# Performance work log

Measured on AMD Instinct MI355X. Metric: run time of the kernel, lower is better.

## Reference

```python
import jax, jax.numpy as jnp
import numpy as np

N_NODES = 16384
N_EDGES = 65536
N_GRAPHS = 64
HID = 768
D = 256       # gnn_hidden_dim == gnn_out_features
HEADS = 4
EPS_LN = 1e-5


def setup_inputs() -> dict:
    key = jax.random.key(0)
    ks = jax.random.split(key, 20)
    s = 0.02
    inp = {
        'text_cls': jax.random.normal(ks[0], (N_GRAPHS, HID), jnp.float32),
        'node_x': jax.random.normal(ks[1], (N_NODES, HID), jnp.float32),
        'node_proj_w': jax.random.normal(ks[2], (HID, D), jnp.float32) * s,
        'node_proj_b': jnp.zeros((D,), jnp.float32),
        # TransformerConv params, stacked over 2 layers. Q/K/V: D -> heads*D
        'Wq': jax.random.normal(ks[3], (2, D, HEADS * D), jnp.float32) * s,
        'bq': jnp.zeros((2, HEADS * D), jnp.float32),
        'Wk': jax.random.normal(ks[4], (2, D, HEADS * D), jnp.float32) * s,
        'bk': jnp.zeros((2, HEADS * D), jnp.float32),
        'Wv': jax.random.normal(ks[5], (2, D, HEADS * D), jnp.float32) * s,
        'bv': jnp.zeros((2, HEADS * D), jnp.float32),
        # root/skip connection: D -> D
        'Ws': jax.random.normal(ks[6], (2, D, D), jnp.float32) * s,
        'bs': jnp.zeros((2, D), jnp.float32),
        # index 0 = gnn_norms[0], index 1 = gnn_last_norm
        'norm_gamma': jnp.ones((2, D), jnp.float32),
        'norm_beta': jnp.zeros((2, D), jnp.float32),
        'clf_w': jax.random.normal(ks[7], (2 * D + HID, 1), jnp.float32) * s,
        'clf_b': jnp.zeros((1,), jnp.float32),
        'edge_index': jax.random.randint(ks[8], (2, N_EDGES), 0, N_NODES, jnp.int32),
        'batch_ids': jnp.sort(jax.random.randint(ks[9], (N_NODES,), 0, N_GRAPHS, jnp.int32)),
    }
    return inp


def _layernorm(x, g, b):
    mu = x.mean(-1, keepdims=True)
    var = ((x - mu) ** 2).mean(-1, keepdims=True)
    return (x - mu) * jax.lax.rsqrt(var + EPS_LN) * g + b


def _transformer_conv(x, src, dst, Wq, bq, Wk, bk, Wv, bv, Ws, bs):
    # PyG TransformerConv: heads=4, concat=False (mean over heads), root_weight=True
    N = x.shape[0]
    q = (x @ Wq + bq).reshape(N, HEADS, D)
    k = (x @ Wk + bk).reshape(N, HEADS, D)
    v = (x @ Wv + bv).reshape(N, HEADS, D)
    qe, ke, ve = q[dst], k[src], v[src]                 # [E, H, D]
    score = (qe * ke).sum(-1) / jnp.sqrt(jnp.float32(D))  # [E, H]
    m = jax.ops.segment_max(score, dst, num_segments=N)
    m = jnp.where(jnp.isfinite(m), m, 0.0)
    ex = jnp.exp(score - m[dst])
    den = jax.ops.segment_sum(ex, dst, num_segments=N)
    alpha = ex / (den[dst] + 1e-16)                     # softmax over in-edges
    agg = jax.ops.segment_sum(alpha[..., None] * ve, dst, num_segments=N)  # [N,H,D]
    return agg.mean(axis=1) + x @ Ws + bs


def reference(text_cls, node_x, node_proj_w, node_proj_b, Wq, bq, Wk, bk, Wv, bv,
              Ws, bs, norm_gamma, norm_beta, clf_w, clf_b, edge_index, batch_ids):
    B = text_cls.shape[0]
    src, dst = edge_index[0], edge_index[1]

    # claim-relevance reweighting (cosine similarity)
    tex = text_cls[batch_ids]                            # [N, 768]
    num = (tex * node_x).sum(-1)
    den = jnp.linalg.norm(tex, axis=-1) * jnp.linalg.norm(node_x, axis=-1)
    rel = num / jnp.maximum(den, 1e-8)
    nf = node_x * rel[:, None]

    x = nf @ node_proj_w + node_proj_b                   # [N, 256]
    for i in range(2):
        h = _transformer_conv(x, src, dst, Wq[i], bq[i], Wk[i], bk[i],
                              Wv[i], bv[i], Ws[i], bs[i])
        if i < 1:
            h = _layernorm(h + x, norm_gamma[i], norm_beta[i])   # residual + LN
        else:
            h = _layernorm(h, norm_gamma[i], norm_beta[i])       # last norm
        x = jax.nn.relu(h)

    # structural mean pool
    counts = jax.ops.segment_sum(jnp.ones((x.shape[0],), x.dtype), batch_ids,
                                 num_segments=B)
    pool_struct = jax.ops.segment_sum(x, batch_ids, num_segments=B) \
        / jnp.maximum(counts, 1.0)[:, None]

    # semantic claim-attention pool (attn_proj is Identity since out==hidden)
    tproj = tex @ node_proj_w + node_proj_b
    scores = (x * tproj).sum(-1)                         # [N]
    ex = jnp.exp(scores)                                 # raw exp, as in source
    denom = jax.ops.segment_sum(ex, batch_ids, num_segments=B)
    aw = ex / (denom[batch_ids] + 1e-8)
    pool_sem = jax.ops.segment_sum(x * aw[:, None], batch_ids, num_segments=B)

    combined = jnp.concatenate([pool_struct, pool_sem, text_cls], axis=-1)
    logits = (combined @ clf_w + clf_b)[:, 0]            # [B]
    return logits
```

## Files before the change

kernel.cpp:

```cpp
#include <hip/hip_runtime.h>

#define N_NODES 16384
#define N_EDGES 65536
#define N_GRAPHS 64
#define HID 768
#define DDIM 256
#define HEADS 4

typedef __attribute__((ext_vector_type(8))) short bf16x8;
typedef __attribute__((ext_vector_type(4))) float f32x4;
typedef __attribute__((ext_vector_type(8))) unsigned short u16x8;

#define GLL(SRC, DST) __builtin_amdgcn_global_load_lds( \
    (const __attribute__((address_space(1))) void*)(SRC), \
    (__attribute__((address_space(3))) void*)(DST), 16, 0, 0)

__device__ __forceinline__ float wave_reduce_sum(float v) {
#pragma unroll
    for (int off = 32; off; off >>= 1) v += __shfl_xor(v, off);
    return v;
}

__device__ __forceinline__ unsigned short f2bf(float f) {
    unsigned u = __float_as_uint(f);
    return (unsigned short)((u + 0x7fffu + ((u >> 16) & 1u)) >> 16);
}
__device__ __forceinline__ float bf2f(unsigned short h) {
    return __uint_as_float((unsigned)h << 16);
}

__global__ __launch_bounds__(256) void relnf_kernel(
        const float* __restrict__ text, const float* __restrict__ nodex,
        const int* __restrict__ bid, unsigned short* __restrict__ nfs) {
    int n = blockIdx.x, t = threadIdx.x;
    const float* xr = nodex + (size_t)n * HID;
    const float* tr = text + (size_t)bid[n] * HID;
    float xv[3];
    float num = 0.f, tt = 0.f, xx = 0.f;
#pragma unroll
    for (int j = 0; j < 3; j++) {
        int c = t + j * 256;
        float a = xr[c], b = tr[c];
        xv[j] = a; num += a * b; tt += b * b; xx += a * a;
    }
    num = wave_reduce_sum(num);
    tt = wave_reduce_sum(tt);
    xx = wave_reduce_sum(xx);
    __shared__ float s0[4], s1[4], s2[4];
    int lane = t & 63, wv = t >> 6;
    if (lane == 0) { s0[wv] = num; s1[wv] = tt; s2[wv] = xx; }
    __syncthreads();
    num = s0[0] + s0[1] + s0[2] + s0[3];
    tt  = s1[0] + s1[1] + s1[2] + s1[3];
    xx  = s2[0] + s2[1] + s2[2] + s2[3];
    float r = num / fmaxf(sqrtf(tt) * sqrtf(xx), 1e-8f);
    unsigned short* o = nfs + (size_t)n * 1536;
#pragma unroll
    for (int j = 0; j < 3; j++) {
        int c = t + j * 256;
        o[c] = f2bf(xv[j] * r);
    }
}

__global__ void wconv_kernel(const float* __restrict__ W, unsigned short* __restrict__ out,
                             int K, int N) {
    int k = blockIdx.x * 256 + threadIdx.x;
    int n = blockIdx.y;
    if (k >= K) return;
    float a = W[(size_t)k * N + n];
    unsigned short h = f2bf(a);
    unsigned short l = f2bf(a - bf2f(h));
    size_t o = (size_t)n * (3 * K);
    out[o + k] = h;
    out[o + K + k] = h;
    out[o + 2 * K + k] = l;
}

__global__ void wprep_kernel(const float* __restrict__ Wq, const float* __restrict__ Wk,
                             const float* __restrict__ Wv, const float* __restrict__ Ws,
                             const float* __restrict__ bq, const float* __restrict__ bk,
                             const float* __restrict__ bv, const float* __restrict__ bs,
                             unsigned short* __restrict__ Wall, float* __restrict__ ballY) {
    __shared__ float red[4];
    int L = blockIdx.y;
    const float* Wk_ = Wk + (size_t)L * DDIM * 1024;
    const float* Wv_ = Wv + (size_t)L * DDIM * 1024;
    const float* Ws_ = Ws + (size_t)L * DDIM * DDIM;
    const float* bq_ = bq + L * 1024;
    const float* bv_ = bv + L * 1024;
    const float* bs_ = bs + L * DDIM;
    unsigned short* Wl = Wall + (size_t)L * 2304 * 256;
    float* bl = ballY + L * 2304;
    int n = blockIdx.x, t = threadIdx.x;
    int lane = t & 63, wv = t >> 6;
    if (n < 1024) {
        Wl[(size_t)(1024 + n) * 256 + t] = f2bf(Wv_[(size_t)t * 1024 + n]);
        if (t == 0) bl[1024 + n] = bv_[n];
    } else if (n < 1280) {
        int col = n - 1024;
        Wl[(size_t)(2048 + col) * 256 + t] = f2bf(Ws_[(size_t)t * 256 + col]);
        if (t == 0) bl[2048 + col] = bs_[col];
    } else {
        int m = n - 1280; int h = m >> 8, b = m & 255;
        float v = Wk_[(size_t)b * 1024 + h * 256 + t] * bq_[h * 256 + t];
        v = wave_reduce_sum(v);
        if (lane == 0) red[wv] = v;
        __syncthreads();
        if (t == 0) bl[m] = red[0] + red[1] + red[2] + red[3];
    }
}

__global__ __launch_bounds__(256, 2) void mker_f32(
        const float* __restrict__ WA, const float* __restrict__ WB,
        unsigned short* __restrict__ Wall) {
    __shared__ unsigned short As_[128 * 64];
    __shared__ unsigned short Bs_[128 * 64];
    const int tid = threadIdx.x;
    const int lane = tid & 63, wave = tid >> 6;
    const int wm = wave >> 1, wn = wave & 1;
    const int row0 = blockIdx.y * 128, col0 = blockIdx.x * 128;
    const int z = blockIdx.z, L = z >> 2, h = z & 3;
    const float* Aq = WA + (size_t)L * DDIM * 1024;
    const float* Ak = WB + (size_t)L * DDIM * 1024;
    unsigned short* Wl = Wall + (size_t)L * 2304 * 256;
    const int l15 = lane & 15, l16 = lane >> 4;
    f32x4 acc[4][4] = {};
    int sr = tid >> 1, scc = (tid & 1) * 32;
    for (int k0 = 0; k0 < 256; k0 += 64) {
        __syncthreads();
        {
            const float* pa = Aq + (size_t)(row0 + sr) * 1024 + h * 256 + k0 + scc;
            const float* pb = Ak + (size_t)(col0 + sr) * 1024 + h * 256 + k0 + scc;
            unsigned short* da = As_ + sr * 64 + scc;
            unsigned short* db = Bs_ + sr * 64 + scc;
#pragma unroll
            for (int j = 0; j < 8; j++) {
                float4 va = ((const float4*)pa)[j];
                float4 vb2 = ((const float4*)pb)[j];
                ((ushort4*)da)[j] = make_ushort4(f2bf(va.x), f2bf(va.y), f2bf(va.z), f2bf(va.w));
                ((ushort4*)db)[j] = make_ushort4(f2bf(vb2.x), f2bf(vb2.y), f2bf(vb2.z), f2bf(vb2.w));
            }
        }
        __syncthreads();
#pragma unroll
        for (int kk = 0; kk < 2; kk++) {
            bf16x8 af[4], bfr[4];
#pragma unroll
            for (int f = 0; f < 4; f++) {
                af[f]  = *(const bf16x8*)(As_ + ((wm * 64 + f * 16 + l15) * 64 + kk * 32 + l16 * 8));
                bfr[f] = *(const bf16x8*)(Bs_ + ((wn * 64 + f * 16 + l15) * 64 + kk * 32 + l16 * 8));
            }
#pragma unroll
            for (int fi = 0; fi < 4; fi++)
#pragma unroll
                for (int fj = 0; fj < 4; fj++)
                    acc[fi][fj] = __builtin_amdgcn_mfma_f32_16x16x32_bf16(
                        af[fi], bfr[fj], acc[fi][fj], 0, 0, 0);
        }
    }
#pragma unroll
    for (int fj = 0; fj < 4; fj++) {
        int cc = col0 + wn * 64 + fj * 16 + l15;
#pragma unroll
        for (int fi = 0; fi < 4; fi++) {
            int rbase = row0 + wm * 64 + fi * 16 + l16 * 4;
#pragma unroll
            for (int r = 0; r < 4; r++)
                Wl[(size_t)(h * 256 + rbase + r) * 256 + cc] = f2bf(acc[fi][fj][r]);
        }
    }
}

__device__ __forceinline__ void swz_block(int& bx, int& by) {
    int nwg = gridDim.x * gridDim.y;
    int lin = blockIdx.y * gridDim.x + blockIdx.x;
    int qd = nwg >> 3, rr = nwg & 7;
    int xcd = lin & 7, j = lin >> 3;
    int wg = (xcd < rr ? xcd * (qd + 1) : rr * (qd + 1) + (xcd - rr) * qd) + j;
    bx = wg % gridDim.x;
    by = wg / gridDim.x;
}

__global__ __launch_bounds__(256, 4) void gemm_proj64(
        const unsigned short* __restrict__ A, const unsigned short* __restrict__ B,
        const float* __restrict__ bias, float* __restrict__ x,
        unsigned short* __restrict__ xb) {
    __shared__ unsigned short As[2][4096];
    __shared__ unsigned short Bs[2][4096];
    int bx, by; swz_block(bx, by);
    const int tid = threadIdx.x;
    const int lane = tid & 63, wave = tid >> 6;
    const int wm = wave >> 1, wn = wave & 1;
    const int row0 = by * 64, col0 = bx * 64;
    const int l15 = lane & 15, l16 = lane >> 4;
    f32x4 acc[2][2] = {};
    const char* Ac = (const char*)A;
    const char* Bc = (const char*)B;

#define PSTAGE(BUF, T) do { \
    int k_ = (T) * 128; \
    _Pragma("unroll") \
    for (int i_ = 0; i_ < 2; i_++) { \
        int o_ = i_ * 4096 + tid * 16; \
        int r_ = o_ >> 7, cb_ = o_ & 127; \
        int cs_ = cb_ ^ ((r_ & 7) << 4); \
        GLL(Ac + (size_t)(row0 + r_) * 3072 + k_ + cs_, (char*)As[BUF] + o_); \
        GLL(Bc + (size_t)(col0 + r_) * 4608 + k_ + cs_, (char*)Bs[BUF] + o_); \
    } } while (0)

#define PCOMPUTE(BUF) do { \
    _Pragma("unroll") \
    for (int kk = 0; kk < 2; kk++) { \
        bf16x8 af[2], bfr[2]; \
        _Pragma("unroll") \
        for (int f = 0; f < 2; f++) { \
            int rowa_ = wm * 32 + f * 16 + l15; \
            int qba_ = (kk * 64 + l16 * 16) ^ ((rowa_ & 7) << 4); \
            af[f]  = *(const bf16x8*)((const char*)As[BUF] + rowa_ * 128 + qba_); \
            int rowb_ = wn * 32 + f * 16 + l15; \
            int qbb_ = (kk * 64 + l16 * 16) ^ ((rowb_ & 7) << 4); \
            bfr[f] = *(const bf16x8*)((const char*)Bs[BUF] + rowb_ * 128 + qbb_); \
        } \
        _Pragma("unroll") \
        for (int fi = 0; fi < 2; fi++) \
            _Pragma("unroll") \
            for (int fj = 0; fj < 2; fj++) \
                acc[fi][fj] = __builtin_amdgcn_mfma_f32_16x16x32_bf16( \
                    af[fi], bfr[fj], acc[fi][fj], 0, 0, 0); \
    } } while (0)

    PSTAGE(0, 0);
    __syncthreads();
    for (int t = 0; t < 12; t += 2) {
        PSTAGE(1, t + 1);
        PCOMPUTE(0); __syncthreads();
        if (t + 2 < 12) PSTAGE(0, t + 2);
        PCOMPUTE(1); __syncthreads();
    }
#undef PSTAGE
#undef PCOMPUTE
    float* smemf = (float*)&As[0][0];
#pragma unroll
    for (int fj = 0; fj < 2; fj++) {
        int cl = wn * 32 + fj * 16 + l15;
        float bb = bias[col0 + cl];
#pragma unroll
        for (int fi = 0; fi < 2; fi++)
#pragma unroll
            for (int r = 0; r < 4; r++) {
                int rl = wm * 32 + fi * 16 + l16 * 4 + r;
                int c16 = cl >> 2;
                smemf[rl * 64 + ((c16 ^ (rl & 15)) << 2) + (cl & 3)] = acc[fi][fj][r] + bb;
            }
    }
    __syncthreads();
    int rl = tid >> 2, q = tid & 3;
#pragma unroll
    for (int i = 0; i < 4; i++) {
        int c16 = q * 4 + i;
        float4 v4 = *(const float4*)&smemf[rl * 64 + ((c16 ^ (rl & 15)) << 2)];
        *(float4*)(x + (size_t)(row0 + rl) * 256 + col0 + c16 * 4) = v4;
        *(ushort4*)(xb + (size_t)(row0 + rl) * 256 + col0 + c16 * 4) =
            make_ushort4(f2bf(v4.x), f2bf(v4.y), f2bf(v4.z), f2bf(v4.w));
    }
}

__global__ __launch_bounds__(256, 6) void gemm_yvs64(
        const unsigned short* __restrict__ A, const unsigned short* __restrict__ B,
        const float* __restrict__ ball,
        unsigned short* __restrict__ Yb, unsigned short* __restrict__ vb,
        unsigned short* __restrict__ hb) {
    __shared__ unsigned short smem[12288];
    unsigned short* As = smem;
    unsigned short* Bs = smem + 4096;
    int bx, by; swz_block(bx, by);
    const int tid = threadIdx.x;
    const int lane = tid & 63, wave = tid >> 6;
    const int wm = wave >> 1, wn = wave & 1;
    const int row0 = by * 64, col0 = bx * 128;
    const int l15 = lane & 15, l16 = lane >> 4;
    f32x4 acc[2][4] = {};
    const char* Ac = (const char*)A;
    const char* Bc = (const char*)B;

    for (int k0 = 0; k0 < 256; k0 += 64) {
        __syncthreads();
#pragma unroll
        for (int i = 0; i < 2; i++) {
            int o = i * 4096 + tid * 16;
            int r = o >> 7, cb = o & 127;
            GLL(Ac + (size_t)(row0 + r) * 512 + k0 * 2 + (cb ^ ((r & 7) << 4)), (char*)As + o);
        }
#pragma unroll
        for (int i = 0; i < 4; i++) {
            int o = i * 4096 + tid * 16;
            int r = o >> 7, cb = o & 127;
            GLL(Bc + (size_t)(col0 + r) * 512 + k0 * 2 + (cb ^ ((r & 7) << 4)), (char*)Bs + o);
        }
        __syncthreads();
#pragma unroll
        for (int kk = 0; kk < 2; kk++) {
            bf16x8 af[2], bfr[4];
#pragma unroll
            for (int f = 0; f < 2; f++) {
                int row = wm * 32 + f * 16 + l15;
                int qb_ = (kk * 64 + l16 * 16) ^ ((row & 7) << 4);
                af[f] = *(const bf16x8*)((const char*)As + row * 128 + qb_);
            }
#pragma unroll
            for (int f = 0; f < 4; f++) {
                int row = wn * 64 + f * 16 + l15;
                int qb_ = (kk * 64 + l16 * 16) ^ ((row & 7) << 4);
                bfr[f] = *(const bf16x8*)((const char*)Bs + row * 128 + qb_);
            }
#pragma unroll
            for (int fi = 0; fi < 2; fi++)
#pragma unroll
                for (int fj = 0; fj < 4; fj++)
                    acc[fi][fj] = __builtin_amdgcn_mfma_f32_16x16x32_bf16(
                        af[fi], bfr[fj], acc[fi][fj], 0, 0, 0);
        }
    }
    __syncthreads();
#pragma unroll
    for (int fj = 0; fj < 4; fj++) {
        int cl = wn * 64 + fj * 16 + l15;
        float bb = ball[col0 + cl];
#pragma unroll
        for (int fi = 0; fi < 2; fi++)
#pragma unroll
            for (int r = 0; r < 4; r++) {
                int rl = wm * 32 + fi * 16 + l16 * 4 + r;
                int chunk = (cl >> 3) ^ (rl & 15);
                smem[rl * 128 + chunk * 8 + (cl & 7)] = f2bf(acc[fi][fj][r] + bb);
            }
    }
    __syncthreads();
    int rl = tid >> 2, part = tid & 3;
    unsigned short* dstp;
    if (col0 < 1024)      dstp = Yb + (size_t)(row0 + rl) * 1024 + col0 + part * 32;
    else if (col0 < 2048) dstp = vb + (size_t)(row0 + rl) * 1024 + (col0 - 1024) + part * 32;
    else                  dstp = hb + (size_t)(row0 + rl) * 256 + (col0 - 2048) + part * 32;
#pragma unroll
    for (int i = 0; i < 4; i++) {
        int chunk = (part * 4 + i) ^ (rl & 15);
        ((u16x8*)dstp)[i] = *(const u16x8*)(smem + rl * 128 + chunk * 8);
    }
}

__global__ __launch_bounds__(256) void tp_kernel(
        const float* __restrict__ text, const float* __restrict__ Wp,
        const float* __restrict__ bp, float* __restrict__ tp64) {
    __shared__ float trow[768];
    int g = blockIdx.x, t = threadIdx.x;
#pragma unroll
    for (int j = 0; j < 3; j++) trow[t + j * 256] = text[(size_t)g * 768 + t + j * 256];
    __syncthreads();
    float acc = bp[t];
#pragma unroll 4
    for (int k = 0; k < 768; k++) acc += trow[k] * Wp[(size_t)k * 256 + t];
    tp64[(size_t)g * 256 + t] = acc;
}

__global__ void hist_kernel(const int* __restrict__ dst, int* __restrict__ cnt) {
    int e = blockIdx.x * 256 + threadIdx.x;
    if (e < N_EDGES) atomicAdd(&cnt[dst[e]], 1);
}

__global__ void scan_kernel(const int* __restrict__ cnt, int* __restrict__ base,
                            int* __restrict__ cursor) {
    int t = threadIdx.x;
    int s = 0;
    for (int i = 0; i < 64; i++) s += cnt[t * 64 + i];
    __shared__ int pref[256];
    pref[t] = s;
    __syncthreads();
    if (t == 0) {
        int a = 0;
        for (int i = 0; i < 256; i++) { int v = pref[i]; pref[i] = a; a += v; }
    }
    __syncthreads();
    int run = pref[t];
    for (int i = 0; i < 64; i++) {
        base[t * 64 + i] = run;
        cursor[t * 64 + i] = run;
        run += cnt[t * 64 + i];
    }
}

__global__ void scatter_kernel(const int* __restrict__ src, const int* __restrict__ dst,
                               int* __restrict__ cursor, int* __restrict__ esrc) {
    int e = blockIdx.x * 256 + threadIdx.x;
    if (e < N_EDGES) {
        int d = dst[e];
        int pos = atomicAdd(&cursor[d], 1);
        esrc[pos] = src[e];
    }
}

__global__ void gbounds_kernel(const int* __restrict__ bid, int* __restrict__ gstart) {
    int g = threadIdx.x;
    if (g > N_GRAPHS) return;
    int lo = 0, hi = N_NODES;
    while (lo < hi) { int mid = (lo + hi) >> 1; if (bid[mid] < g) lo = mid + 1; else hi = mid; }
    gstart[g] = lo;
}

template<bool RESID, bool WXB>
__global__ __launch_bounds__(256) void agg_norm_fused(
        const unsigned short* __restrict__ vb, const unsigned short* __restrict__ Yb,
        const int* __restrict__ base, const int* __restrict__ cnt,
        const int* __restrict__ esrc, const unsigned short* __restrict__ hb,
        float* __restrict__ x, const unsigned short* __restrict__ xin,
        unsigned short* __restrict__ xout,
        const float* __restrict__ gamma, const float* __restrict__ beta) {
    __shared__ float hacc[4][256];
    __shared__ float tmp[4];
    int n = (blockIdx.x & 7) * (N_NODES >> 3) + (blockIdx.x >> 3);
    int tid = threadIdx.x, lane = tid & 63, h = tid >> 6;
    int start = base[n], deg = cnt[n];

    ushort4 ya = ((const ushort4*)(Yb + (size_t)n * 1024 + h * 256))[lane];
    float y0 = bf2f(ya.x), y1 = bf2f(ya.y), y2 = bf2f(ya.z), y3 = bf2f(ya.w);

    float m0 = -1e30f, den0 = 0.f, m1 = -1e30f, den1 = 0.f;
    float4 acc0 = {0.f, 0.f, 0.f, 0.f}, acc1 = {0.f, 0.f, 0.f, 0.f};
    ushort4 xsA = {0, 0, 0, 0}, vvA = {0, 0, 0, 0};
    ushort4 xsB = {0, 0, 0, 0}, vvB = {0, 0, 0, 0};
    if (deg > 0) {
        int s = esrc[start];
        xsA = ((const ushort4*)(xin + (size_t)s * 256))[lane];
        vvA = ((const ushort4*)(vb + (size_t)s * 1024 + h * 256))[lane];
    }
    if (deg > 1) {
        int s = esrc[start + 1];
        xsB = ((const ushort4*)(xin + (size_t)s * 256))[lane];
        vvB = ((const ushort4*)(vb + (size_t)s * 1024 + h * 256))[lane];
    }
    for (int i = 0; i < deg; i += 2) {
        ushort4 xsA_n = xsA, vvA_n = vvA, xsB_n = xsB, vvB_n = vvB;
        if (i + 2 < deg) {
            int s = esrc[start + i + 2];
            xsA_n = ((const ushort4*)(xin + (size_t)s * 256))[lane];
            vvA_n = ((const ushort4*)(vb + (size_t)s * 1024 + h * 256))[lane];
        }
        if (i + 3 < deg) {
            int s = esrc[start + i + 3];
            xsB_n = ((const ushort4*)(xin + (size_t)s * 256))[lane];
            vvB_n = ((const ushort4*)(vb + (size_t)s * 1024 + h * 256))[lane];
        }
        float p0 = y0 * bf2f(xsA.x) + y1 * bf2f(xsA.y)
                 + y2 * bf2f(xsA.z) + y3 * bf2f(xsA.w);
        float p1 = y0 * bf2f(xsB.x) + y1 * bf2f(xsB.y)
                 + y2 * bf2f(xsB.z) + y3 * bf2f(xsB.w);
#pragma unroll
        for (int off = 32; off; off >>= 1) {
            p0 += __shfl_xor(p0, off);
            p1 += __shfl_xor(p1, off);
        }
        p0 *= 0.0625f; p1 *= 0.0625f;
        if (p0 > m0) {
            float sc_ = __expf(m0 - p0);
            den0 = den0 * sc_ + 1.0f;
            acc0.x = acc0.x * sc_ + bf2f(vvA.x);
            acc0.y = acc0.y * sc_ + bf2f(vvA.y);
            acc0.z = acc0.z * sc_ + bf2f(vvA.z);
            acc0.w = acc0.w * sc_ + bf2f(vvA.w);
            m0 = p0;
        } else {
            float a = __expf(p0 - m0);
            den0 += a;
            acc0.x += a * bf2f(vvA.x); acc0.y += a * bf2f(vvA.y);
            acc0.z += a * bf2f(vvA.z); acc0.w += a * bf2f(vvA.w);
        }
        if (i + 1 < deg) {
            if (p1 > m1) {
                float sc_ = __expf(m1 - p1);
                den1 = den1 * sc_ + 1.0f;
                acc1.x = acc1.x * sc_ + bf2f(vvB.x);
                acc1.y = acc1.y * sc_ + bf2f(vvB.y);
                acc1.z = acc1.z * sc_ + bf2f(vvB.z);
                acc1.w = acc1.w * sc_ + bf2f(vvB.w);
                m1 = p1;
            } else {
                float a = __expf(p1 - m1);
                den1 += a;
                acc1.x += a * bf2f(vvB.x); acc1.y += a * bf2f(vvB.y);
                acc1.z += a * bf2f(vvB.z); acc1.w += a * bf2f(vvB.w);
            }
        }
        xsA = xsA_n; vvA = vvA_n; xsB = xsB_n; vvB = vvB_n;
    }
    float mm = fmaxf(m0, m1);
    float e0 = __expf(m0 - mm), e1 = __expf(m1 - mm);
    float den = den0 * e0 + den1 * e1;
    float4 acc;
    acc.x = acc0.x * e0 + acc1.x * e1;
    acc.y = acc0.y * e0 + acc1.y * e1;
    acc.z = acc0.z * e0 + acc1.z * e1;
    acc.w = acc0.w * e0 + acc1.w * e1;
    float inv_den = 0.25f / (den + 1e-16f);
    acc.x *= inv_den; acc.y *= inv_den; acc.z *= inv_den; acc.w *= inv_den;
    ((float4*)&hacc[h][lane * 4])[0] = acc;
    __syncthreads();

    int c = tid;
    float val = hacc[0][c] + hacc[1][c] + hacc[2][c] + hacc[3][c]
              + bf2f(hb[(size_t)n * 256 + c]);
    if (RESID) val += x[(size_t)n * 256 + c];

    float s1 = wave_reduce_sum(val);
    if (lane == 0) tmp[h] = s1;
    __syncthreads();
    float mu = (tmp[0] + tmp[1] + tmp[2] + tmp[3]) * (1.0f / 256.0f);
    __syncthreads();
    float d = val - mu;
    float s2 = wave_reduce_sum(d * d);
    if (lane == 0) tmp[h] = s2;
    __syncthreads();
    float inv = rsqrtf((tmp[0] + tmp[1] + tmp[2] + tmp[3]) * (1.0f / 256.0f) + 1e-5f);
    float o = fmaxf(d * inv * gamma[c] + beta[c], 0.f);
    x[(size_t)n * 256 + c] = o;
    if (WXB) xout[(size_t)n * 256 + c] = f2bf(o);
}

__global__ __launch_bounds__(256) void pool_seg(
        const float* __restrict__ x, const float* __restrict__ tp,
        const int* __restrict__ gstart, float* __restrict__ pstruct,
        float* __restrict__ psem, float* __restrict__ semden) {
    int g = blockIdx.x >> 2, q = blockIdx.x & 3;
    int s0 = gstart[g], s1 = gstart[g + 1];
    int chunk = (s1 - s0 + 3) >> 2;
    int a = s0 + q * chunk, b = min(a + chunk, s1);
    int wave = threadIdx.x >> 6, lane = threadIdx.x & 63;
    float4 tv = ((const float4*)(tp + (size_t)g * 256))[lane];
    float4 acc = {0.f, 0.f, 0.f, 0.f};
    float4 accs = {0.f, 0.f, 0.f, 0.f};
    float esum = 0.f;
    for (int n = a + wave; n < b; n += 4) {
        float4 xv = ((const float4*)(x + (size_t)n * 256))[lane];
        float p = wave_reduce_sum(xv.x * tv.x + xv.y * tv.y + xv.z * tv.z + xv.w * tv.w);
        float e = __expf(p);
        esum += e;
        acc.x += xv.x; acc.y += xv.y; acc.z += xv.z; acc.w += xv.w;
        accs.x += e * xv.x; accs.y += e * xv.y; accs.z += e * xv.z; accs.w += e * xv.w;
    }
    __shared__ float sacc[4][256];
    __shared__ float sacc2[4][256];
    __shared__ float tse[4];
    ((float4*)&sacc[wave][lane * 4])[0] = acc;
    ((float4*)&sacc2[wave][lane * 4])[0] = accs;
    if (lane == 0) tse[wave] = esum;
    __syncthreads();
    int c = threadIdx.x;
    float v = sacc[0][c] + sacc[1][c] + sacc[2][c] + sacc[3][c];
    float v2 = sacc2[0][c] + sacc2[1][c] + sacc2[2][c] + sacc2[3][c];
    atomicAdd(&pstruct[(size_t)g * 256 + c], v);
    atomicAdd(&psem[(size_t)g * 256 + c], v2);
    if (threadIdx.x == 0)
        atomicAdd(&semden[g], tse[0] + tse[1] + tse[2] + tse[3]);
}

__global__ void clf_kernel(const float* __restrict__ pstruct, const float* __restrict__ psem,
                           const float* __restrict__ semden,
                           const int* __restrict__ gstart, const float* __restrict__ text,
                           const float* __restrict__ w, const float* __restrict__ b,
                           float* __restrict__ out) {
    int g = blockIdx.x * 4 + (threadIdx.x >> 6);
    int lane = threadIdx.x & 63;
    float invc = 1.0f / fmaxf((float)(gstart[g + 1] - gstart[g]), 1.0f);
    float invs = 1.0f / (semden[g] + 1e-8f);
    float acc = 0.f;
#pragma unroll
    for (int i = 0; i < 4; i++) { int c = lane + i * 64; acc += pstruct[(size_t)g * 256 + c] * invc * w[c]; }
#pragma unroll
    for (int i = 0; i < 4; i++) { int c = lane + i * 64; acc += psem[(size_t)g * 256 + c] * invs * w[256 + c]; }
#pragma unroll
    for (int i = 0; i < 12; i++) { int c = lane + i * 64; acc += text[(size_t)g * 768 + c] * w[512 + c]; }
    acc = wave_reduce_sum(acc);
    if (lane == 0) out[g] = acc + b[0];
}

extern "C" void kernel_launch(void* const* d_in, const int* in_sizes, int n_in,
                              void* d_out, int out_size, void* d_ws, size_t ws_size,
                              hipStream_t stream) {
    const float* text  = (const float*)d_in[0];
    const float* nodex = (const float*)d_in[1];
    const float* Wp    = (const float*)d_in[2];
    const float* bp    = (const float*)d_in[3];
    const float* Wq    = (const float*)d_in[4];
    const float* bq    = (const float*)d_in[5];
    const float* Wk    = (const float*)d_in[6];
    const float* bk    = (const float*)d_in[7];
    const float* Wv    = (const float*)d_in[8];
    const float* bv    = (const float*)d_in[9];
    const float* Ws    = (const float*)d_in[10];
    const float* bs    = (const float*)d_in[11];
    const float* gamma = (const float*)d_in[12];
    const float* beta  = (const float*)d_in[13];
    const float* clfw  = (const float*)d_in[14];
    const float* clfb  = (const float*)d_in[15];
    const int*   eidx  = (const int*)d_in[16];
    const int*   bid   = (const int*)d_in[17];
    const int* src = eidx;
    const int* dst = eidx + N_EDGES;
    float* out = (float*)d_out;

    float* x     = (float*)d_ws;
    float* tp64  = x + (size_t)N_NODES * 256;
    float* pstruct = tp64 + 64 * 256;
    float* psem  = pstruct + 64 * 256;
    float* semden = psem + 64 * 256;
    float* ballY = semden + 64;
    int* esrc    = (int*)(ballY + 2 * 2304);
    int* cnt     = esrc + N_EDGES;
    int* base    = cnt + N_NODES;
    int* cursor  = base + N_NODES;
    int* gstart  = cursor + N_NODES;
    unsigned short* Yb   = (unsigned short*)(gstart + 80);
    unsigned short* vb   = Yb + (size_t)N_NODES * 1024;
    unsigned short* hb   = vb + (size_t)N_NODES * 1024;
    unsigned short* xb   = hb + (size_t)N_NODES * 256;
    unsigned short* xb2  = xb + (size_t)N_NODES * 256;
    unsigned short* Wall = xb2 + (size_t)N_NODES * 256;
    unsigned short* Wps  = Wall + (size_t)2 * 2304 * 256;
    unsigned short* nfs = Yb;

    relnf_kernel<<<N_NODES, 256, 0, stream>>>(text, nodex, bid, nfs);
    hipMemsetAsync(cnt, 0, N_NODES * sizeof(int), stream);
    hist_kernel<<<N_EDGES / 256, 256, 0, stream>>>(dst, cnt);
    scan_kernel<<<1, 256, 0, stream>>>(cnt, base, cursor);
    scatter_kernel<<<N_EDGES / 256, 256, 0, stream>>>(src, dst, cursor, esrc);
    gbounds_kernel<<<1, 128, 0, stream>>>(bid, gstart);

    wconv_kernel<<<dim3(HID / 256, DDIM), 256, 0, stream>>>(Wp, Wps, HID, DDIM);
    wprep_kernel<<<dim3(2304, 2), 256, 0, stream>>>(Wq, Wk, Wv, Ws, bq, bk, bv, bs,
                                                    Wall, ballY);
    mker_f32<<<dim3(2, 2, 8), 256, 0, stream>>>(Wk, Wq, Wall);

    gemm_proj64<<<dim3(DDIM / 64, N_NODES / 64), 256, 0, stream>>>(nfs, Wps, bp, x, xb);
    tp_kernel<<<N_GRAPHS, 256, 0, stream>>>(text, Wp, bp, tp64);

    for (int i = 0; i < 2; i++) {
        const unsigned short* xin = (i == 0) ? xb : xb2;
        gemm_yvs64<<<dim3(18, N_NODES / 64), 256, 0, stream>>>(
            xin, Wall + (size_t)i * 2304 * 256, ballY + i * 2304, Yb, vb, hb);
        if (i == 0)
            agg_norm_fused<true, true><<<N_NODES, 256, 0, stream>>>(
                vb, Yb, base, cnt, esrc, hb, x, xin, xb2, gamma, beta);
        else
            agg_norm_fused<false, false><<<N_NODES, 256, 0, stream>>>(
                vb, Yb, base, cnt, esrc, hb, x, xin, xb2, gamma + 256, beta + 256);
    }

    hipMemsetAsync(pstruct, 0, (size_t)(64 * 256 * 2 + 64) * sizeof(float), stream);
    pool_seg<<<N_GRAPHS * 4, 256, 0, stream>>>(x, tp64, gstart, pstruct, psem, semden);
    clf_kernel<<<N_GRAPHS / 4, 256, 0, stream>>>(pstruct, psem, semden, gstart, text,
                                                 clfw, clfb, out);
}
```

Measured before the change: 336.7 us.

## Merge weight-prep, text projection and memsets into one launch; fold histogram into relnf

Replaces the wconv, wprep, mker, tp kernels and two memsets with a single prep_mega launch that branches on block index. The edge-degree histogram moves into relnf_kernel (each node block adds four edges' counts), and the graph-bounds search moves into scan_kernel. This cuts the number of launches and their small-kernel tail overhead. The cost is a heterogeneous mega-kernel whose register and LDS footprint is set by the MFMA branch, which may limit occupancy for the simple branches.

```diff
diff --git a/kernel.cpp b/kernel.cpp
--- a/kernel.cpp
+++ b/kernel.cpp
@@ -31,8 +31,10 @@
 
 __global__ __launch_bounds__(256) void relnf_kernel(
         const float* __restrict__ text, const float* __restrict__ nodex,
-        const int* __restrict__ bid, unsigned short* __restrict__ nfs) {
+        const int* __restrict__ bid, const int* __restrict__ dst,
+        unsigned short* __restrict__ nfs, int* __restrict__ cnt) {
     int n = blockIdx.x, t = threadIdx.x;
+    if (t < 4) atomicAdd(&cnt[dst[4 * n + t]], 1);
     const float* xr = nodex + (size_t)n * HID;
     const float* tr = text + (size_t)bid[n] * HID;
     float xv[3];
@@ -62,112 +64,163 @@
     }
 }
 
-__global__ void wconv_kernel(const float* __restrict__ W, unsigned short* __restrict__ out,
-                             int K, int N) {
-    int k = blockIdx.x * 256 + threadIdx.x;
-    int n = blockIdx.y;
-    if (k >= K) return;
-    float a = W[(size_t)k * N + n];
-    unsigned short h = f2bf(a);
-    unsigned short l = f2bf(a - bf2f(h));
-    size_t o = (size_t)n * (3 * K);
-    out[o + k] = h;
-    out[o + K + k] = h;
-    out[o + 2 * K + k] = l;
-}
-
-__global__ void wprep_kernel(const float* __restrict__ Wq, const float* __restrict__ Wk,
-                             const float* __restrict__ Wv, const float* __restrict__ Ws,
-                             const float* __restrict__ bq, const float* __restrict__ bk,
-                             const float* __restrict__ bv, const float* __restrict__ bs,
-                             unsigned short* __restrict__ Wall, float* __restrict__ ballY) {
-    __shared__ float red[4];
-    int L = blockIdx.y;
-    const float* Wk_ = Wk + (size_t)L * DDIM * 1024;
-    const float* Wv_ = Wv + (size_t)L * DDIM * 1024;
-    const float* Ws_ = Ws + (size_t)L * DDIM * DDIM;
-    const float* bq_ = bq + L * 1024;
-    const float* bv_ = bv + L * 1024;
-    const float* bs_ = bs + L * DDIM;
-    unsigned short* Wl = Wall + (size_t)L * 2304 * 256;
-    float* bl = ballY + L * 2304;
-    int n = blockIdx.x, t = threadIdx.x;
-    int lane = t & 63, wv = t >> 6;
-    if (n < 1024) {
-        Wl[(size_t)(1024 + n) * 256 + t] = f2bf(Wv_[(size_t)t * 1024 + n]);
-        if (t == 0) bl[1024 + n] = bv_[n];
-    } else if (n < 1280) {
-        int col = n - 1024;
-        Wl[(size_t)(2048 + col) * 256 + t] = f2bf(Ws_[(size_t)t * 256 + col]);
-        if (t == 0) bl[2048 + col] = bs_[col];
-    } else {
-        int m = n - 1280; int h = m >> 8, b = m & 255;
-        float v = Wk_[(size_t)b * 1024 + h * 256 + t] * bq_[h * 256 + t];
-        v = wave_reduce_sum(v);
-        if (lane == 0) red[wv] = v;
-        __syncthreads();
-        if (t == 0) bl[m] = red[0] + red[1] + red[2] + red[3];
-    }
-}
-
-__global__ __launch_bounds__(256, 2) void mker_f32(
-        const float* __restrict__ WA, const float* __restrict__ WB,
-        unsigned short* __restrict__ Wall) {
+__global__ __launch_bounds__(256, 2) void prep_mega(
+        const float* __restrict__ Wp, const float* __restrict__ Wq,
+        const float* __restrict__ Wk, const float* __restrict__ Wv,
+        const float* __restrict__ Ws, const float* __restrict__ bq,
+        const float* __restrict__ bk, const float* __restrict__ bv,
+        const float* __restrict__ bs, const float* __restrict__ text,
+        const float* __restrict__ bp,
+        unsigned short* __restrict__ Wps, unsigned short* __restrict__ Wall,
+        float* __restrict__ ballY, float* __restrict__ tp64,
+        int* __restrict__ cnt, float* __restrict__ pzero) {
     __shared__ unsigned short As_[128 * 64];
     __shared__ unsigned short Bs_[128 * 64];
-    const int tid = threadIdx.x;
-    const int lane = tid & 63, wave = tid >> 6;
-    const int wm = wave >> 1, wn = wave & 1;
-    const int row0 = blockIdx.y * 128, col0 = blockIdx.x * 128;
-    const int z = blockIdx.z, L = z >> 2, h = z & 3;
-    const float* Aq = WA + (size_t)L * DDIM * 1024;
-    const float* Ak = WB + (size_t)L * DDIM * 1024;
-    unsigned short* Wl = Wall + (size_t)L * 2304 * 256;
-    const int l15 = lane & 15, l16 = lane >> 4;
-    f32x4 acc[4][4] = {};
-    int sr = tid >> 1, scc = (tid & 1) * 32;
-    for (int k0 = 0; k0 < 256; k0 += 64) {
+    const int b = blockIdx.x, t = threadIdx.x;
+    if (b < 768) {
+        int k = (b % 3) * 256 + t, n = b / 3;
+        float a = Wp[(size_t)k * 256 + n];
+        unsigned short h = f2bf(a), l = f2bf(a - bf2f(h));
+        size_t o = (size_t)n * 2304;
+        Wps[o + k] = h; Wps[o + 768 + k] = h; Wps[o + 1536 + k] = l;
+    } else if (b < 5376) {
+        float* red = (float*)As_;
+        int m = b - 768;
+        int n = m % 2304, L = m / 2304;
+        const float* Wk_ = Wk + (size_t)L * DDIM * 1024;
+        const float* Wv_ = Wv + (size_t)L * DDIM * 1024;
+        const float* Ws_ = Ws + (size_t)L * DDIM * DDIM;
+        const float* bq_ = bq + L * 1024;
+        const float* bv_ = bv + L * 1024;
+        const float* bs_ = bs + L * DDIM;
+        unsigned short* Wl = Wall + (size_t)L * 2304 * 256;
+        float* bl = ballY + L * 2304;
+        int lane = t & 63, wv = t >> 6;
+        if (n < 1024) {
+            Wl[(size_t)(1024 + n) * 256 + t] = f2bf(Wv_[(size_t)t * 1024 + n]);
+            if (t == 0) bl[1024 + n] = bv_[n];
+        } else if (n < 1280) {
+            int col = n - 1024;
+            Wl[(size_t)(2048 + col) * 256 + t] = f2bf(Ws_[(size_t)t * 256 + col]);
+            if (t == 0) bl[2048 + col] = bs_[col];
+        } else {
+            int mm = n - 1280; int h = mm >> 8, bcol = mm & 255;
+            float v = Wk_[(size_t)bcol * 1024 + h * 256 + t] * bq_[h * 256 + t];
+            v = wave_reduce_sum(v);
+            if (lane == 0) red[wv] = v;
+            __syncthreads();
+            if (t == 0) bl[mm] = red[0] + red[1] + red[2] + red[3];
+        }
+    } else if (b < 5408) {
+        int m = b - 5376;
+        const int bx = m & 1, by = (m >> 1) & 1, z = m >> 2;
+        const int L = z >> 2, h = z & 3;
+        const int lane = t & 63, wave = t >> 6;
+        const int wm = wave >> 1, wn = wave & 1;
+        const int row0 = by * 128, col0 = bx * 128;
+        const float* Aq = Wk + (size_t)L * DDIM * 1024;
+        const float* Ak = Wq + (size_t)L * DDIM * 1024;
+        unsigned short* Wl = Wall + (size_t)L * 2304 * 256;
+        const int l15 = lane & 15, l16 = lane >> 4;
+        f32x4 acc[4][4] = {};
+        int sr = t >> 1, scc = (t & 1) * 32;
+        for (int k0 = 0; k0 < 256; k0 += 64) {
+            __syncthreads();
+            {
+                const float* pa = Aq + (size_t)(row0 + sr) * 1024 + h * 256 + k0 + scc;
+                const float* pb = Ak + (size_t)(col0 + sr) * 1024 + h * 256 + k0 + scc;
+                unsigned short* da = As_ + sr * 64 + scc;
+                unsigned short* db = Bs_ + sr * 64 + scc;
+#pragma unroll
+                for (int j = 0; j < 8; j++) {
+                    float4 va = ((const float4*)pa)[j];
+                    float4 vb2 = ((const float4*)pb)[j];
+                    ((ushort4*)da)[j] = make_ushort4(f2bf(va.x), f2bf(va.y), f2bf(va.z), f2bf(va.w));
+                    ((ushort4*)db)[j] = make_ushort4(f2bf(vb2.x), f2bf(vb2.y), f2bf(vb2.z), f2bf(vb2.w));
+                }
+            }
+            __syncthreads();
+#pragma unroll
+            for (int kk = 0; kk < 2; kk++) {
+                bf16x8 af[4], bfr[4];
+#pragma unroll
+                for (int f = 0; f < 4; f++) {
+                    af[f]  = *(const bf16x8*)(As_ + ((wm * 64 + f * 16 + l15) * 64 + kk * 32 + l16 * 8));
+                    bfr[f] = *(const bf16x8*)(Bs_ + ((wn * 64 + f * 16 + l15) * 64 + kk * 32 + l16 * 8));
+                }
+#pragma unroll
+                for (int fi = 0; fi < 4; fi++)
+#pragma unroll
+                    for (int fj = 0; fj < 4; fj++)
+                        acc[fi][fj] = __builtin_amdgcn_mfma_f32_16x16x32_bf16(
+                            af[fi], bfr[fj], acc[fi][fj], 0, 0, 0);
+            }
+        }
+#pragma unroll
+        for (int fj = 0; fj < 4; fj++) {
+            int cc = col0 + wn * 64 + fj * 16 + l15;
+#pragma unroll
+            for (int fi = 0; fi < 4; fi++) {
+                int rbase = row0 + wm * 64 + fi * 16 + l16 * 4;
+#pragma unroll
+                for (int r = 0; r < 4; r++)
+                    Wl[(size_t)(h * 256 + rbase + r) * 256 + cc] = f2bf(acc[fi][fj][r]);
+            }
+        }
+    } else if (b < 5472) {
+        float* trow = (float*)As_;
+        int g = b - 5408;
+#pragma unroll
+        for (int j = 0; j < 3; j++) trow[t + j * 256] = text[(size_t)g * 768 + t + j * 256];
         __syncthreads();
-        {
-            const float* pa = Aq + (size_t)(row0 + sr) * 1024 + h * 256 + k0 + scc;
-            const float* pb = Ak + (size_t)(col0 + sr) * 1024 + h * 256 + k0 + scc;
-            unsigned short* da = As_ + sr * 64 + scc;
-            unsigned short* db = Bs_ + sr * 64 + scc;
-#pragma unroll
-            for (int j = 0; j < 8; j++) {
-                float4 va = ((const float4*)pa)[j];
-                float4 vb2 = ((const float4*)pb)[j];
-                ((ushort4*)da)[j] = make_ushort4(f2bf(va.x), f2bf(va.y), f2bf(va.z), f2bf(va.w));
-                ((ushort4*)db)[j] = make_ushort4(f2bf(vb2.x), f2bf(vb2.y), f2bf(vb2.z), f2bf(vb2.w));
-            }
-        }
-        __syncthreads();
-#pragma unroll
-        for (int kk = 0; kk < 2; kk++) {
-            bf16x8 af[4], bfr[4];
-#pragma unroll
-            for (int f = 0; f < 4; f++) {
-                af[f]  = *(const bf16x8*)(As_ + ((wm * 64 + f * 16 + l15) * 64 + kk * 32 + l16 * 8));
-                bfr[f] = *(const bf16x8*)(Bs_ + ((wn * 64 + f * 16 + l15) * 64 + kk * 32 + l16 * 8));
-            }
-#pragma unroll
-            for (int fi = 0; fi < 4; fi++)
-#pragma unroll
-                for (int fj = 0; fj < 4; fj++)
-                    acc[fi][fj] = __builtin_amdgcn_mfma_f32_16x16x32_bf16(
-                        af[fi], bfr[fj], acc[fi][fj], 0, 0, 0);
-        }
-    }
-#pragma unroll
-    for (int fj = 0; fj < 4; fj++) {
-        int cc = col0 + wn * 64 + fj * 16 + l15;
-#pragma unroll
-        for (int fi = 0; fi < 4; fi++) {
-            int rbase = row0 + wm * 64 + fi * 16 + l16 * 4;
-#pragma unroll
-            for (int r = 0; r < 4; r++)
-                Wl[(size_t)(h * 256 + rbase + r) * 256 + cc] = f2bf(acc[fi][fj][r]);
-        }
+        float acc = bp[t];
+#pragma unroll 4
+        for (int k = 0; k < 768; k++) acc += trow[k] * Wp[(size_t)k * 256 + t];
+        tp64[(size_t)g * 256 + t] = acc;
+    } else if (b < 5488) {
+        int i = (b - 5472) * 1024 + t * 4;
+        ((int4*)(cnt + i))[0] = make_int4(0, 0, 0, 0);
+    } else {
+        int i = (b - 5488) * 1024 + t * 4;
+        if (i < 32832)
+            ((float4*)(pzero + i))[0] = make_float4(0.f, 0.f, 0.f, 0.f);
+    }
+}
+
+__global__ void scan_kernel(const int* __restrict__ cnt, int* __restrict__ base,
+                            int* __restrict__ cursor, const int* __restrict__ bid,
+                            int* __restrict__ gstart) {
+    int t = threadIdx.x;
+    if (t <= 64) {
+        int lo = 0, hi = N_NODES;
+        while (lo < hi) { int mid = (lo + hi) >> 1; if (bid[mid] < t) lo = mid + 1; else hi = mid; }
+        gstart[t] = lo;
+    }
+    int s = 0;
+    for (int i = 0; i < 64; i++) s += cnt[t * 64 + i];
+    __shared__ int pref[256];
+    pref[t] = s;
+    __syncthreads();
+    if (t == 0) {
+        int a = 0;
+        for (int i = 0; i < 256; i++) { int v = pref[i]; pref[i] = a; a += v; }
+    }
+    __syncthreads();
+    int run = pref[t];
+    for (int i = 0; i < 64; i++) {
+        base[t * 64 + i] = run;
+        cursor[t * 64 + i] = run;
+        run += cnt[t * 64 + i];
+    }
+}
+
+__global__ void scatter_kernel(const int* __restrict__ src, const int* __restrict__ dst,
+                               int* __restrict__ cursor, int* __restrict__ esrc) {
+    int e = blockIdx.x * 256 + threadIdx.x;
+    if (e < N_EDGES) {
+        int d = dst[e];
+        int pos = atomicAdd(&cursor[d], 1);
+        esrc[pos] = src[e];
     }
 }
 
@@ -346,64 +399,6 @@
         int chunk = (part * 4 + i) ^ (rl & 15);
         ((u16x8*)dstp)[i] = *(const u16x8*)(smem + rl * 128 + chunk * 8);
     }
-}
-
-__global__ __launch_bounds__(256) void tp_kernel(
-        const float* __restrict__ text, const float* __restrict__ Wp,
-        const float* __restrict__ bp, float* __restrict__ tp64) {
-    __shared__ float trow[768];
-    int g = blockIdx.x, t = threadIdx.x;
-#pragma unroll
-    for (int j = 0; j < 3; j++) trow[t + j * 256] = text[(size_t)g * 768 + t + j * 256];
-    __syncthreads();
-    float acc = bp[t];
-#pragma unroll 4
-    for (int k = 0; k < 768; k++) acc += trow[k] * Wp[(size_t)k * 256 + t];
-    tp64[(size_t)g * 256 + t] = acc;
-}
-
-__global__ void hist_kernel(const int* __restrict__ dst, int* __restrict__ cnt) {
-    int e = blockIdx.x * 256 + threadIdx.x;
-    if (e < N_EDGES) atomicAdd(&cnt[dst[e]], 1);
-}
-
-__global__ void scan_kernel(const int* __restrict__ cnt, int* __restrict__ base,
-                            int* __restrict__ cursor) {
-    int t = threadIdx.x;
-    int s = 0;
-    for (int i = 0; i < 64; i++) s += cnt[t * 64 + i];
-    __shared__ int pref[256];
-    pref[t] = s;
-    __syncthreads();
-    if (t == 0) {
-        int a = 0;
-        for (int i = 0; i < 256; i++) { int v = pref[i]; pref[i] = a; a += v; }
-    }
-    __syncthreads();
-    int run = pref[t];
-    for (int i = 0; i < 64; i++) {
-        base[t * 64 + i] = run;
-        cursor[t * 64 + i] = run;
-        run += cnt[t * 64 + i];
-    }
-}
-
-__global__ void scatter_kernel(const int* __restrict__ src, const int* __restrict__ dst,
-                               int* __restrict__ cursor, int* __restrict__ esrc) {
-    int e = blockIdx.x * 256 + threadIdx.x;
-    if (e < N_EDGES) {
-        int d = dst[e];
-        int pos = atomicAdd(&cursor[d], 1);
-        esrc[pos] = src[e];
-    }
-}
-
-__global__ void gbounds_kernel(const int* __restrict__ bid, int* __restrict__ gstart) {
-    int g = threadIdx.x;
-    if (g > N_GRAPHS) return;
-    int lo = 0, hi = N_NODES;
-    while (lo < hi) { int mid = (lo + hi) >> 1; if (bid[mid] < g) lo = mid + 1; else hi = mid; }
-    gstart[g] = lo;
 }
 
 template<bool RESID, bool WXB>
@@ -626,20 +621,13 @@
     unsigned short* Wps  = Wall + (size_t)2 * 2304 * 256;
     unsigned short* nfs = Yb;
 
-    relnf_kernel<<<N_NODES, 256, 0, stream>>>(text, nodex, bid, nfs);
-    hipMemsetAsync(cnt, 0, N_NODES * sizeof(int), stream);
-    hist_kernel<<<N_EDGES / 256, 256, 0, stream>>>(dst, cnt);
-    scan_kernel<<<1, 256, 0, stream>>>(cnt, base, cursor);
+    prep_mega<<<5521, 256, 0, stream>>>(Wp, Wq, Wk, Wv, Ws, bq, bk, bv, bs, text, bp,
+                                        Wps, Wall, ballY, tp64, cnt, pstruct);
+    relnf_kernel<<<N_NODES, 256, 0, stream>>>(text, nodex, bid, dst, nfs, cnt);
+    scan_kernel<<<1, 256, 0, stream>>>(cnt, base, cursor, bid, gstart);
     scatter_kernel<<<N_EDGES / 256, 256, 0, stream>>>(src, dst, cursor, esrc);
-    gbounds_kernel<<<1, 128, 0, stream>>>(bid, gstart);
-
-    wconv_kernel<<<dim3(HID / 256, DDIM), 256, 0, stream>>>(Wp, Wps, HID, DDIM);
-    wprep_kernel<<<dim3(2304, 2), 256, 0, stream>>>(Wq, Wk, Wv, Ws, bq, bk, bv, bs,
-                                                    Wall, ballY);
-    mker_f32<<<dim3(2, 2, 8), 256, 0, stream>>>(Wk, Wq, Wall);
 
     gemm_proj64<<<dim3(DDIM / 64, N_NODES / 64), 256, 0, stream>>>(nfs, Wps, bp, x, xb);
-    tp_kernel<<<N_GRAPHS, 256, 0, stream>>>(text, Wp, bp, tp64);
 
     for (int i = 0; i < 2; i++) {
         const unsigned short* xin = (i == 0) ? xb : xb2;
@@ -653,7 +641,6 @@
                 vb, Yb, base, cnt, esrc, hb, x, xin, xb2, gamma + 256, beta + 256);
     }
 
-    hipMemsetAsync(pstruct, 0, (size_t)(64 * 256 * 2 + 64) * sizeof(float), stream);
     pool_seg<<<N_GRAPHS * 4, 256, 0, stream>>>(x, tp64, gstart, pstruct, psem, semden);
     clf_kernel<<<N_GRAPHS / 4, 256, 0, stream>>>(pstruct, psem, semden, gstart, text,
                                                  clfw, clfb, out);
```

Result: faster. 309.0 us (-8.2%).
